# Kernel tuning notes

Measured on AMD Instinct MI355X. Metric: run time of the kernel, lower is better.

Reference implementation:

```python
import jax, jax.numpy as jnp
import numpy as np

D = 128          # embed_dim
NSYM = 100000    # num_symbols
PAD = NSYM       # padding index
DM = 2 * D       # d_model for support/query encoders
HID = 2 * DM     # LSTMCell hidden size
STEPS = 4        # process_steps
K_NEI = 10       # k_neighbors
EPS = 1e-8
LN_EPS = 1e-5
SLOPE = 0.01     # F.leaky_relu default negative slope


def _neighbor_encoder(conn, num_neighbors, self_ids, sym_emb, gcn_w_W, gcn_w_b, gcn_b, gate_w, gate_temp):
    rel = conn[..., 0]                      # [N, K]
    ent = conn[..., 1]                      # [N, K]
    rel_e = sym_emb[rel]                    # [N, K, D]  (dropout is identity in eval)
    ent_e = sym_emb[ent]                    # [N, K, D]
    self_e = sym_emb[self_ids]              # [N, D]
    concat = jnp.concatenate([rel_e, ent_e], axis=-1)                 # [N, K, 2D]
    proj = jax.nn.leaky_relu(concat @ gcn_w_W.T + gcn_w_b + gcn_b, SLOPE)
    proj = proj * (rel != PAD)[..., None].astype(proj.dtype)          # zero padded slots
    d = D // 2
    rs, is_ = self_e[:, None, :d], self_e[:, None, d:]
    rn, in_ = proj[..., :d], proj[..., d:]
    num = jnp.sum(rs * rn, -1) + jnp.sum(is_ * in_, -1)               # [N, K]
    n_self = jnp.sqrt(jnp.sum(rs * rs + is_ * is_, -1) + EPS)
    n_nei = jnp.sqrt(jnp.sum(rn * rn + in_ * in_, -1) + EPS)
    cos = num / (n_self * n_nei + EPS)
    _, idx = jax.lax.top_k(cos, K_NEI)                                # [N, k]
    agg = jnp.take_along_axis(proj, idx[..., None], axis=1).mean(axis=1)   # [N, D]
    rel_ids = jnp.where(rel == PAD, 0, rel)
    gate = jax.nn.sigmoid(gate_w[rel_ids, 0].mean(axis=1, keepdims=True) / gate_temp)  # [N, 1]
    gate = jnp.where(num_neighbors[:, None] > 0, gate, jnp.ones_like(gate))
    return jnp.tanh(self_e + gate * agg)


def _support_encoder(x, W1, b1, W2, b2, g, b):
    # FFN with residual + LayerNorm (dropout = identity in eval)
    h = jax.nn.relu(x @ W1.T + b1) @ W2.T + b2 + x
    mu = h.mean(-1, keepdims=True)
    var = ((h - mu) ** 2).mean(-1, keepdims=True)
    return g * (h - mu) / jnp.sqrt(var + LN_EPS) + b


def _query_encoder(support, query, Wih, Whh, bih, bhh):
    # Matching-network process block: LSTMCell attention over support
    B = query.shape[0]
    h_r = jnp.zeros((B, HID), query.dtype)
    c = jnp.zeros((B, HID), query.dtype)
    h = query
    for _ in range(STEPS):  # small fixed loop
        gates = query @ Wih.T + bih + h_r @ Whh.T + bhh
        i, f, g, o = jnp.split(gates, 4, axis=-1)
        c = jax.nn.sigmoid(f) * c + jax.nn.sigmoid(i) * jnp.tanh(g)
        h_new = jax.nn.sigmoid(o) * jnp.tanh(c)
        h = query + h_new[:, :DM]
        attn = jax.nn.softmax(h @ support.T, axis=1)
        r = attn @ support
        h_r = jnp.concatenate([h, r], axis=1)
    return h


def _forward(query, support, q_l1, q_deg_l, q_r1, q_deg_r, s_l1, s_deg_l, s_r1, s_deg_r, p):
    ne = lambda conn, deg, ids: _neighbor_encoder(conn, deg, ids, p['sym_emb'], p['gcn_w_W'], p['gcn_w_b'], p['gcn_b'], p['gate_w'], p['gate_temp'])
    q_vec = jnp.concatenate([ne(q_l1, q_deg_l, query[:, 0]), ne(q_r1, q_deg_r, query[:, 1])], -1)   # [B, DM]
    s_vec = jnp.concatenate([ne(s_l1, s_deg_l, support[:, 0]), ne(s_r1, s_deg_r, support[:, 1])], -1)
    se = lambda x: _support_encoder(x, p['se_W1'], p['se_b1'], p['se_W2'], p['se_b2'], p['ln_g'], p['ln_b'])
    support_g = se(s_vec).mean(axis=0, keepdims=True)   # [1, DM]
    query_enc = se(q_vec)                                # [B, DM]
    query_g = _query_encoder(support_g, query_enc, p['lstm_Wih'], p['lstm_Whh'], p['lstm_bih'], p['lstm_bhh'])
    d = DM // 2
    rq, iq = query_g[..., :d], query_g[..., d:]
    rs, is_ = support_g[..., :d], support_g[..., d:]
    num = jnp.sum(rq * rs, -1) + jnp.sum(iq * is_, -1)
    den = jnp.sqrt(jnp.sum(rq * rq + iq * iq, -1) + EPS) * jnp.sqrt(jnp.sum(rs * rs + is_ * is_, -1) + EPS)
    return num / den  # [B]


def setup_inputs():
    key = jax.random.key(0)
    ks = jax.random.split(key, 24)
    B, FEW, MAXK = 4096, 5, 50
    ri = lambda k, shp, hi: jax.random.randint(k, shp, 0, hi)
    inp = dict(
        query=ri(ks[0], (B, 2), NSYM),
        support=ri(ks[1], (FEW, 2), NSYM),
        q_l1=ri(ks[2], (B, MAXK, 2), NSYM + 1),
        q_deg_l=ri(ks[3], (B,), MAXK),
        q_r1=ri(ks[4], (B, MAXK, 2), NSYM + 1),
        q_deg_r=ri(ks[5], (B,), MAXK),
        s_l1=ri(ks[6], (FEW, MAXK, 2), NSYM + 1),
        s_deg_l=ri(ks[7], (FEW,), MAXK),
        s_r1=ri(ks[8], (FEW, MAXK, 2), NSYM + 1),
        s_deg_r=ri(ks[9], (FEW,), MAXK),
    )
    xav = lambda k, shp: jax.random.normal(k, shp) * np.float32(np.sqrt(2.0 / (shp[0] + shp[1])))
    sym = jax.random.normal(ks[10], (NSYM + 1, D)) * 0.02
    inp['sym_emb'] = sym.at[PAD].set(0.0)
    inp['gcn_w_W'] = xav(ks[11], (D, 2 * D))
    inp['gcn_w_b'] = jnp.zeros((D,))
    inp['gcn_b'] = jnp.zeros((D,))
    inp['gate_w'] = 1.0 + 0.05 * jax.random.normal(ks[12], (NSYM, 1))
    inp['gate_temp'] = jnp.asarray(1.0, jnp.float32)
    inp['se_W1'] = xav(ks[13], (2 * DM, DM))
    inp['se_b1'] = jnp.zeros((2 * DM,))
    inp['se_W2'] = xav(ks[14], (DM, 2 * DM))
    inp['se_b2'] = jnp.zeros((DM,))
    inp['ln_g'] = jnp.ones((DM,))
    inp['ln_b'] = jnp.zeros((DM,))
    s = float(1.0 / np.sqrt(HID))
    u = lambda k, shp: jax.random.uniform(k, shp, minval=-s, maxval=s)
    inp['lstm_Wih'] = u(ks[15], (4 * HID, DM))
    inp['lstm_Whh'] = u(ks[16], (4 * HID, HID))
    inp['lstm_bih'] = u(ks[17], (4 * HID,))
    inp['lstm_bhh'] = u(ks[18], (4 * HID,))
    return inp


def reference(query, support, q_l1, q_deg_l, q_r1, q_deg_r, s_l1, s_deg_l, s_r1, s_deg_r,
              sym_emb, gcn_w_W, gcn_w_b, gcn_b, gate_w, gate_temp,
              se_W1, se_b1, se_W2, se_b2, ln_g, ln_b,
              lstm_Wih, lstm_Whh, lstm_bih, lstm_bhh):
    p = dict(sym_emb=sym_emb, gcn_w_W=gcn_w_W, gcn_w_b=gcn_w_b, gcn_b=gcn_b, gate_w=gate_w,
             gate_temp=gate_temp, se_W1=se_W1, se_b1=se_b1, se_W2=se_W2, se_b2=se_b2,
             ln_g=ln_g, ln_b=ln_b, lstm_Wih=lstm_Wih, lstm_Whh=lstm_Whh, lstm_bih=lstm_bih, lstm_bhh=lstm_bhh)
    return _forward(query, support, q_l1, q_deg_l, q_r1, q_deg_r, s_l1, s_deg_l, s_r1, s_deg_r, p)
```

## Files before the change

### kernel.cpp

```cpp
#include <hip/hip_runtime.h>

#define PADID  100000
#define DEPS   1e-8f
#define LNEPS  1e-5f

typedef unsigned short u16;
typedef unsigned int u32;
typedef __attribute__((ext_vector_type(8))) short s16x8;
typedef __attribute__((ext_vector_type(4))) float f32x4;

__device__ __forceinline__ float sigm(float x) { return 1.f / (1.f + expf(-x)); }
__device__ __forceinline__ float bf2f(u16 v) { return __uint_as_float(((u32)v) << 16); }
__device__ __forceinline__ u16 f2bf(float f) {
    u32 x = __float_as_uint(f);
    x += 0x7FFFu + ((x >> 16) & 1u);
    return (u16)(x >> 16);
}

__global__ void transpose_f32(const float* __restrict__ src, float* __restrict__ dst,
                              int R, int C) {
    int idx = blockIdx.x * 256 + threadIdx.x;
    if (idx < R * C) {
        int r = idx / C, c = idx - r * C;
        dst[c * R + r] = src[idx];
    }
}

__global__ __launch_bounds__(256) void ne_kernel(
    const float* __restrict__ sym, const float* __restrict__ wT,
    const float* __restrict__ wbias, const float* __restrict__ gbias,
    const float* __restrict__ gate_w, const float* __restrict__ gtemp,
    const int* __restrict__ query, const int* __restrict__ support,
    const int* __restrict__ q_l1, const int* __restrict__ q_r1,
    const int* __restrict__ s_l1, const int* __restrict__ s_r1,
    const int* __restrict__ q_deg_l, const int* __restrict__ q_deg_r,
    const int* __restrict__ s_deg_l, const int* __restrict__ s_deg_r,
    float* __restrict__ qvec, float* __restrict__ svec)
{
    const int bid  = blockIdx.x;
    const int row  = bid >> 1;
    const int side = bid & 1;
    const int t    = threadIdx.x;
    const int tk   = t & 15;
    const int tj   = t >> 4;

    const int* conn; int selfid, deg; float* out;
    if (row < 4096) {
        conn   = (side ? q_r1 : q_l1) + row * 100;
        deg    = (side ? q_deg_r : q_deg_l)[row];
        selfid = query[row * 2 + side];
        out    = qvec + row * 256 + side * 128;
    } else {
        int r  = row - 4096;
        conn   = (side ? s_r1 : s_l1) + r * 100;
        deg    = (side ? s_deg_r : s_deg_l)[r];
        selfid = support[r * 2 + side];
        out    = svec + r * 256 + side * 128;
    }

    __shared__ float s_nei[64][66];
    __shared__ float s_agg[16][132];
    __shared__ int   s_rel[50], s_ent[50];
    __shared__ float s_self[128];
    __shared__ float s_cos[64];
    __shared__ int   s_topk[10];
    __shared__ float s_misc[2];

    if (t < 50) { s_rel[t] = conn[2 * t]; s_ent[t] = conn[2 * t + 1]; }
    if (t < 128) s_self[t] = sym[(size_t)selfid * 128 + t];
    __syncthreads();

    float sf[8];
    #pragma unroll
    for (int e = 0; e < 8; ++e) sf[e] = s_self[tk * 8 + e];
    if (t < 64) {
        float a = s_self[t], b = s_self[t + 64];
        float s2 = a * a + b * b;
        #pragma unroll
        for (int off = 32; off; off >>= 1) s2 += __shfl_xor(s2, off);
        if (t == 0) s_misc[0] = s2;
    }

    float acc[4][8];
    #pragma unroll
    for (int m = 0; m < 4; ++m)
        #pragma unroll
        for (int e = 0; e < 8; ++e) acc[m][e] = 0.f;

    for (int c = 0; c < 4; ++c) {
        for (int idx = t; idx < 64 * 16; idx += 256) {
            int j = idx >> 4, k4 = (idx & 15) * 4;
            float4 v = make_float4(0.f, 0.f, 0.f, 0.f);
            if (j < 50) {
                int kin = c * 64 + k4;
                int id  = (kin < 128) ? s_rel[j] : s_ent[j];
                v = *(const float4*)&sym[(size_t)id * 128 + (kin & 127)];
            }
            *(float4*)&s_nei[j][k4] = v;
        }
        __syncthreads();
        #pragma unroll 2
        for (int k2 = 0; k2 < 64; ++k2) {
            const float* wrow = wT + (size_t)(c * 64 + k2) * 128 + tk * 8;
            float4 wv0 = *(const float4*)wrow;
            float4 wv1 = *(const float4*)(wrow + 4);
            float wv[8] = {wv0.x, wv0.y, wv0.z, wv0.w, wv1.x, wv1.y, wv1.z, wv1.w};
            #pragma unroll
            for (int m = 0; m < 4; ++m) {
                float nv = s_nei[tj + m * 16][k2];
                #pragma unroll
                for (int e = 0; e < 8; ++e) acc[m][e] += nv * wv[e];
            }
        }
        __syncthreads();
    }

    float wsum[8];
    #pragma unroll
    for (int e = 0; e < 8; ++e) {
        int k = tk * 8 + e;
        wsum[e] = wbias[k] + gbias[k];
    }
    #pragma unroll
    for (int m = 0; m < 4; ++m) {
        int j = tj + m * 16;
        bool dead = (j >= 50) || (s_rel[j < 50 ? j : 0] == PADID && j < 50);
        #pragma unroll
        for (int e = 0; e < 8; ++e) {
            float v = acc[m][e] + wsum[e];
            v = (v > 0.f) ? v : 0.01f * v;
            acc[m][e] = dead ? 0.f : v;
        }
    }

    {
        float ns = sqrtf(s_misc[0] + DEPS);
        #pragma unroll
        for (int m = 0; m < 4; ++m) {
            float num = 0.f, nn = 0.f;
            #pragma unroll
            for (int e = 0; e < 8; ++e) {
                float pv = acc[m][e];
                num += pv * sf[e];
                nn  += pv * pv;
            }
            #pragma unroll
            for (int off = 1; off < 16; off <<= 1) {
                num += __shfl_xor(num, off);
                nn  += __shfl_xor(nn,  off);
            }
            if (tk == 0) {
                int j = tj + m * 16;
                if (j < 50) s_cos[j] = num / (ns * sqrtf(nn + DEPS) + DEPS);
            }
        }
    }
    __syncthreads();

    if (t < 64) {
        float myv  = (t < 50) ? s_cos[t] : -3.4e38f;
        int   live = (t < 50) ? 1 : 0;
        for (int m = 0; m < 10; ++m) {
            float bv = live ? myv : -3.4e38f;
            int   bi = t;
            #pragma unroll
            for (int off = 1; off < 64; off <<= 1) {
                float ov = __shfl_xor(bv, off);
                int   oi = __shfl_xor(bi, off);
                if (ov > bv || (ov == bv && oi < bi)) { bv = ov; bi = oi; }
            }
            if (bi == t) live = 0;
            if (t == 0) s_topk[m] = bi;
        }
        float g = 0.f;
        if (t < 50) {
            int r = s_rel[t];
            g = gate_w[(r == PADID) ? 0 : r];
        }
        #pragma unroll
        for (int off = 32; off; off >>= 1) g += __shfl_xor(g, off);
        if (t == 0) {
            float gate = sigm((g / 50.f) / gtemp[0]);
            if (deg <= 0) gate = 1.f;
            s_misc[1] = gate;
        }
    }
    __syncthreads();

    {
        float ag[8];
        #pragma unroll
        for (int e = 0; e < 8; ++e) ag[e] = 0.f;
        #pragma unroll
        for (int m = 0; m < 4; ++m) {
            int j = tj + m * 16;
            bool sel = false;
            #pragma unroll
            for (int m2 = 0; m2 < 10; ++m2) sel |= (s_topk[m2] == j);
            if (sel)
                #pragma unroll
                for (int e = 0; e < 8; ++e) ag[e] += acc[m][e];
        }
        *(float4*)&s_agg[tj][tk * 8]     = make_float4(ag[0], ag[1], ag[2], ag[3]);
        *(float4*)&s_agg[tj][tk * 8 + 4] = make_float4(ag[4], ag[5], ag[6], ag[7]);
    }
    __syncthreads();

    if (t < 128) {
        float a = 0.f;
        #pragma unroll
        for (int r = 0; r < 16; ++r) a += s_agg[r][t];
        a *= 0.1f;
        out[t] = tanhf(s_self[t] + s_misc[1] * a);
    }
}

#define SE_ROWS 4
__global__ __launch_bounds__(256) void se_kernel(
    const float* __restrict__ qvec, const float* __restrict__ svec,
    const float* __restrict__ w1T, const float* __restrict__ w2T,
    const float* __restrict__ b1, const float* __restrict__ b2,
    const float* __restrict__ lng, const float* __restrict__ lnb,
    float* __restrict__ qenc, float* __restrict__ senc)
{
    const int t  = threadIdx.x;
    const int r0 = blockIdx.x * SE_ROWS;

    __shared__ float sx[SE_ROWS][256];
    __shared__ float shid[SE_ROWS][512];
    __shared__ float sred[4][SE_ROWS][2];

    for (int idx = t; idx < SE_ROWS * 64; idx += 256) {
        int r = idx >> 6, k4 = (idx & 63) * 4;
        int row = r0 + r;
        float4 v = make_float4(0.f, 0.f, 0.f, 0.f);
        if (row < 4101) {
            const float* x = (row < 4096) ? (qvec + (size_t)row * 256)
                                          : (svec + (size_t)(row - 4096) * 256);
            v = *(const float4*)&x[k4];
        }
        *(float4*)&sx[r][k4] = v;
    }
    __syncthreads();

    float h[2][SE_ROWS];
    {
        float bb0 = b1[t], bb1 = b1[t + 256];
        #pragma unroll
        for (int r = 0; r < SE_ROWS; ++r) { h[0][r] = bb0; h[1][r] = bb1; }
    }
    for (int k = 0; k < 256; ++k) {
        float w0 = w1T[k * 512 + t];
        float w1 = w1T[k * 512 + t + 256];
        #pragma unroll
        for (int r = 0; r < SE_ROWS; ++r) {
            float xv = sx[r][k];
            h[0][r] += xv * w0;
            h[1][r] += xv * w1;
        }
    }
    #pragma unroll
    for (int r = 0; r < SE_ROWS; ++r) {
        shid[r][t]       = fmaxf(h[0][r], 0.f);
        shid[r][t + 256] = fmaxf(h[1][r], 0.f);
    }
    __syncthreads();

    float acc2[SE_ROWS];
    {
        float bb = b2[t];
        #pragma unroll
        for (int r = 0; r < SE_ROWS; ++r) acc2[r] = bb + sx[r][t];
    }
    for (int k = 0; k < 512; ++k) {
        float w = w2T[k * 256 + t];
        #pragma unroll
        for (int r = 0; r < SE_ROWS; ++r) acc2[r] += shid[r][k] * w;
    }

    int wv = t >> 6;
    #pragma unroll
    for (int r = 0; r < SE_ROWS; ++r) {
        float s = acc2[r], q = acc2[r] * acc2[r];
        #pragma unroll
        for (int off = 32; off; off >>= 1) {
            s += __shfl_xor(s, off);
            q += __shfl_xor(q, off);
        }
        if ((t & 63) == 0) { sred[wv][r][0] = s; sred[wv][r][1] = q; }
    }
    __syncthreads();
    float gv = lng[t], bv = lnb[t];
    #pragma unroll
    for (int r = 0; r < SE_ROWS; ++r) {
        int row = r0 + r;
        if (row < 4101) {
            float S = sred[0][r][0] + sred[1][r][0] + sred[2][r][0] + sred[3][r][0];
            float Q = sred[0][r][1] + sred[1][r][1] + sred[2][r][1] + sred[3][r][1];
            float mu  = S / 256.f;
            float var = Q / 256.f - mu * mu;
            float o = gv * (acc2[r] - mu) / sqrtf(var + LNEPS) + bv;
            float* op = (row < 4096) ? (qenc + (size_t)row * 256)
                                     : (senc + (size_t)(row - 4096) * 256);
            op[t] = o;
        }
    }
}

__global__ __launch_bounds__(256) void supg_kernel(
    const float* __restrict__ senc, float* __restrict__ supg,
    float* __restrict__ ssqp)
{
    int t = threadIdx.x;
    __shared__ float sr[4];
    float m = (senc[t] + senc[256 + t] + senc[512 + t] + senc[768 + t] + senc[1024 + t]) * 0.2f;
    supg[t] = m;
    float sq = m * m;
    #pragma unroll
    for (int off = 32; off; off >>= 1) sq += __shfl_xor(sq, off);
    if ((t & 63) == 0) sr[t >> 6] = sq;
    __syncthreads();
    if (t == 0) ssqp[0] = sr[0] + sr[1] + sr[2] + sr[3];
}

__global__ __launch_bounds__(256) void supc_kernel(
    const float* __restrict__ supg, const float* __restrict__ Whh,
    const float* __restrict__ bih, const float* __restrict__ bhh,
    float* __restrict__ supc0, float* __restrict__ supc)
{
    const int t = threadIdx.x, w = t >> 6, l = t & 63;
    __shared__ float sg[256];
    if (t < 256) sg[t] = supg[t];
    __syncthreads();
    float4 gv = *(const float4*)&sg[l * 4];
    #pragma unroll
    for (int jj = 0; jj < 16; ++jj) {
        int j = blockIdx.x * 64 + w * 16 + jj;
        float4 wv = *(const float4*)&Whh[(size_t)j * 512 + 256 + l * 4];
        float p = gv.x * wv.x + gv.y * wv.y + gv.z * wv.z + gv.w * wv.w;
        #pragma unroll
        for (int off = 32; off; off >>= 1) p += __shfl_xor(p, off);
        if (l == 0) {
            float c0 = bih[j] + bhh[j];
            supc0[j] = c0;
            supc[j]  = c0 + p;
        }
    }
}

__global__ __launch_bounds__(256) void prep_kernel(
    const float* __restrict__ qenc, const float* __restrict__ Wih,
    const float* __restrict__ Whh, u16* __restrict__ Abf, u16* __restrict__ Wcat)
{
    int idx = blockIdx.x * 256 + threadIdx.x;
    if (idx < 1048576) {
        int m = idx >> 8, k = idx & 255;
        Abf[(size_t)m * 512 + k] = f2bf(qenc[idx]);
    } else if (idx < 1572864) {
        int i = idx - 1048576;
        int n = i >> 8, k = i & 255;
        Wcat[(size_t)n * 512 + k] = f2bf(Wih[i]);
    } else {
        int i = idx - 1572864;
        int n = i >> 8, k = i & 255;
        Wcat[(size_t)n * 512 + 256 + k] = f2bf(Whh[(size_t)n * 512 + k]);
    }
}

__global__ __launch_bounds__(256) void lstm_mfma(
    const u16* __restrict__ A, const u16* __restrict__ B,
    u16* __restrict__ C, int Klen)
{
    __shared__ u16 sA[64][72];
    __shared__ u16 sB[64][72];
    const int t    = threadIdx.x;
    const int wid  = t >> 6;
    const int lane = t & 63;
    const int m0   = blockIdx.x * 64;
    const int n0   = blockIdx.y * 64;
    const int mw   = (wid & 1) * 32;
    const int nw   = (wid >> 1) * 32;
    const int r    = t >> 2;
    const int q    = t & 3;
    const int fr   = lane & 15;
    const int fk   = (lane >> 4) * 8;

    f32x4 acc[2][2];
    #pragma unroll
    for (int i = 0; i < 2; ++i)
        #pragma unroll
        for (int j = 0; j < 2; ++j)
            acc[i][j] = (f32x4){0.f, 0.f, 0.f, 0.f};

    for (int k0 = 0; k0 < Klen; k0 += 64) {
        const u16* ga = A + (size_t)(m0 + r) * 512 + k0 + q * 16;
        const u16* gb = B + (size_t)(n0 + r) * 512 + k0 + q * 16;
        uint4 va0 = *(const uint4*)ga;
        uint4 va1 = *(const uint4*)(ga + 8);
        uint4 vb0 = *(const uint4*)gb;
        uint4 vb1 = *(const uint4*)(gb + 8);
        __syncthreads();
        *(uint4*)&sA[r][q * 16]     = va0;
        *(uint4*)&sA[r][q * 16 + 8] = va1;
        *(uint4*)&sB[r][q * 16]     = vb0;
        *(uint4*)&sB[r][q * 16 + 8] = vb1;
        __syncthreads();
        #pragma unroll
        for (int ks = 0; ks < 64; ks += 32) {
            s16x8 af[2], bf[2];
            #pragma unroll
            for (int i = 0; i < 2; ++i)
                af[i] = *(const s16x8*)&sA[mw + i * 16 + fr][ks + fk];
            #pragma unroll
            for (int j = 0; j < 2; ++j)
                bf[j] = *(const s16x8*)&sB[nw + j * 16 + fr][ks + fk];
            #pragma unroll
            for (int i = 0; i < 2; ++i)
                #pragma unroll
                for (int j = 0; j < 2; ++j)
                    acc[i][j] = __builtin_amdgcn_mfma_f32_16x16x32_bf16(
                        af[i], bf[j], acc[i][j], 0, 0, 0);
        }
    }

    #pragma unroll
    for (int i = 0; i < 2; ++i)
        #pragma unroll
        for (int j = 0; j < 2; ++j) {
            int col = n0 + nw + j * 16 + fr;
            #pragma unroll
            for (int rr = 0; rr < 4; ++rr) {
                int rowi = m0 + mw + i * 16 + (lane >> 4) * 4 + rr;
                C[(size_t)rowi * 2048 + col] = f2bf(acc[i][j][rr]);
            }
        }
}

__global__ __launch_bounds__(256) void lstm_elem(
    const u16* __restrict__ gates, const float* __restrict__ cvec,
    float* __restrict__ cbuf, const float* __restrict__ qenc,
    u16* __restrict__ Abf, float* __restrict__ hfinal, int step)
{
    int idx = blockIdx.x * 256 + threadIdx.x;
    int m = idx >> 9, j = idx & 511;
    const u16* g = gates + (size_t)m * 2048;
    float iv = bf2f(g[j])        + cvec[j];
    float fv = bf2f(g[512 + j])  + cvec[512 + j];
    float gv = bf2f(g[1024 + j]) + cvec[1024 + j];
    float ov = bf2f(g[1536 + j]) + cvec[1536 + j];
    float cold = (step == 0) ? 0.f : cbuf[idx];
    float cn = sigm(fv) * cold + sigm(iv) * tanhf(gv);
    cbuf[idx] = cn;
    if (j < 256) {
        float hn = sigm(ov) * tanhf(cn);
        float h  = qenc[(size_t)m * 256 + j] + hn;
        Abf[(size_t)m * 512 + 256 + j] = f2bf(h);
        if (step == 3) hfinal[(size_t)m * 256 + j] = h;
    }
}

__global__ __launch_bounds__(256) void final_kernel(
    const float* __restrict__ h, const float* __restrict__ supg,
    const float* __restrict__ ssqp, float* __restrict__ outp)
{
    int t = threadIdx.x;
    int w = t >> 6, l = t & 63;
    int b = blockIdx.x * 4 + w;
    float4 q = *(const float4*)&h[b * 256 + l * 4];
    float4 s = *(const float4*)&supg[l * 4];
    float num = q.x * s.x + q.y * s.y + q.z * s.z + q.w * s.w;
    float qq  = q.x * q.x + q.y * q.y + q.z * q.z + q.w * q.w;
    #pragma unroll
    for (int off = 32; off; off >>= 1) {
        num += __shfl_xor(num, off);
        qq  += __shfl_xor(qq,  off);
    }
    if (l == 0) {
        float den = sqrtf(qq + DEPS) * sqrtf(ssqp[0] + DEPS);
        outp[b] = num / den;
    }
}

extern "C" void kernel_launch(void* const* d_in, const int* in_sizes, int n_in,
                              void* d_out, int out_size, void* d_ws, size_t ws_size,
                              hipStream_t stream) {
    const int* query      = (const int*)d_in[0];
    const int* support    = (const int*)d_in[1];
    const int* q_l1       = (const int*)d_in[2];
    const int* q_deg_l    = (const int*)d_in[3];
    const int* q_r1       = (const int*)d_in[4];
    const int* q_deg_r    = (const int*)d_in[5];
    const int* s_l1       = (const int*)d_in[6];
    const int* s_deg_l    = (const int*)d_in[7];
    const int* s_r1       = (const int*)d_in[8];
    const int* s_deg_r    = (const int*)d_in[9];
    const float* sym      = (const float*)d_in[10];
    const float* gcn_w_W  = (const float*)d_in[11];
    const float* gcn_w_b  = (const float*)d_in[12];
    const float* gcn_b    = (const float*)d_in[13];
    const float* gate_w   = (const float*)d_in[14];
    const float* gtemp    = (const float*)d_in[15];
    const float* se_W1    = (const float*)d_in[16];
    const float* se_b1    = (const float*)d_in[17];
    const float* se_W2    = (const float*)d_in[18];
    const float* se_b2    = (const float*)d_in[19];
    const float* ln_g     = (const float*)d_in[20];
    const float* ln_b     = (const float*)d_in[21];
    const float* lstm_Wih = (const float*)d_in[22];
    const float* lstm_Whh = (const float*)d_in[23];
    const float* lstm_bih = (const float*)d_in[24];
    const float* lstm_bhh = (const float*)d_in[25];

    float* ws    = (float*)d_ws;
    float* qvec  = ws;
    float* qenc  = qvec  + 1048576;
    float* h1    = qenc  + 1048576;
    float* cbuf  = h1    + 1048576;
    float* svec  = cbuf  + 2097152;
    float* senc  = svec  + 1280;
    float* supg  = senc  + 1280;
    float* supc0 = supg  + 256;
    float* supc  = supc0 + 2048;
    float* ssqp  = supc  + 2048;
    float* wT    = h1;
    float* w1T   = h1 + 32768;
    float* w2T   = h1 + 163840;
    float* h0    = qvec;
    float* bfbase = ssqp + 64;
    u16* Abf  = (u16*)bfbase;
    u16* Wcat = Abf + 2097152;
    u16* gates= Wcat + 1048576;

    transpose_f32<<<128, 256, 0, stream>>>(gcn_w_W, wT, 128, 256);
    transpose_f32<<<512, 256, 0, stream>>>(se_W1, w1T, 512, 256);
    transpose_f32<<<512, 256, 0, stream>>>(se_W2, w2T, 256, 512);

    ne_kernel<<<8202, 256, 0, stream>>>(
        sym, wT, gcn_w_b, gcn_b, gate_w, gtemp,
        query, support, q_l1, q_r1, s_l1, s_r1,
        q_deg_l, q_deg_r, s_deg_l, s_deg_r, qvec, svec);

    se_kernel<<<1026, 256, 0, stream>>>(
        qvec, svec, w1T, w2T, se_b1, se_b2, ln_g, ln_b, qenc, senc);

    prep_kernel<<<8192, 256, 0, stream>>>(qenc, lstm_Wih, lstm_Whh, Abf, Wcat);
    supg_kernel<<<1, 256, 0, stream>>>(senc, supg, ssqp);
    supc_kernel<<<32, 256, 0, stream>>>(supg, lstm_Whh, lstm_bih, lstm_bhh, supc0, supc);

    for (int s = 0; s < 4; ++s) {
        lstm_mfma<<<dim3(64, 32), 256, 0, stream>>>(Abf, Wcat, gates, s == 0 ? 256 : 512);
        lstm_elem<<<8192, 256, 0, stream>>>(gates, s == 0 ? supc0 : supc,
                                            cbuf, qenc, Abf, h0, s);
    }

    final_kernel<<<1024, 256, 0, stream>>>(h0, supg, ssqp, (float*)d_out);
}
```

Before: 847.1 us.

## Move neighbor-encoder projection onto bf16 MFMA with three-way split precision

Replaces the scalar FP32 GEMM in the neighbor encoder with MFMA bf16 instructions. Both the gathered embeddings and the weights are split into high, mid and low bf16 parts, and six cross-products are summed to approximate FP32 accuracy. Each block now handles two entity rows (128 neighbor slots) and uses a swizzled LDS layout. The weight split is precomputed by a new kernel. The change targets the FP32 ALU cost of the projection, at the price of extra conversion work and more LDS, which may lower occupancy.

```diff
diff --git a/kernel.cpp b/kernel.cpp
--- a/kernel.cpp
+++ b/kernel.cpp
@@ -26,8 +26,20 @@
     }
 }
 
-__global__ __launch_bounds__(256) void ne_kernel(
-    const float* __restrict__ sym, const float* __restrict__ wT,
+__global__ void wsplit_kernel(const float* __restrict__ W, u16* __restrict__ wh,
+                              u16* __restrict__ wm, u16* __restrict__ wl) {
+    int idx = blockIdx.x * 256 + threadIdx.x;
+    float x = W[idx];
+    u16 h = f2bf(x);  float hf = __uint_as_float((u32)h << 16);
+    float r1 = x - hf;
+    u16 m = f2bf(r1); float mf = __uint_as_float((u32)m << 16);
+    u16 l2 = f2bf(r1 - mf);
+    wh[idx] = h; wm[idx] = m; wl[idx] = l2;
+}
+
+__global__ __launch_bounds__(256) void ne_mfma(
+    const float* __restrict__ sym,
+    const u16* __restrict__ wh, const u16* __restrict__ wm, const u16* __restrict__ wl,
     const float* __restrict__ wbias, const float* __restrict__ gbias,
     const float* __restrict__ gate_w, const float* __restrict__ gtemp,
     const int* __restrict__ query, const int* __restrict__ support,
@@ -37,181 +49,265 @@
     const int* __restrict__ s_deg_l, const int* __restrict__ s_deg_r,
     float* __restrict__ qvec, float* __restrict__ svec)
 {
-    const int bid  = blockIdx.x;
-    const int row  = bid >> 1;
-    const int side = bid & 1;
-    const int t    = threadIdx.x;
-    const int tk   = t & 15;
-    const int tj   = t >> 4;
-
-    const int* conn; int selfid, deg; float* out;
-    if (row < 4096) {
-        conn   = (side ? q_r1 : q_l1) + row * 100;
-        deg    = (side ? q_deg_r : q_deg_l)[row];
-        selfid = query[row * 2 + side];
-        out    = qvec + row * 256 + side * 128;
-    } else {
-        int r  = row - 4096;
-        conn   = (side ? s_r1 : s_l1) + r * 100;
-        deg    = (side ? s_deg_r : s_deg_l)[r];
-        selfid = support[r * 2 + side];
-        out    = svec + r * 256 + side * 128;
-    }
-
-    __shared__ float s_nei[64][66];
-    __shared__ float s_agg[16][132];
-    __shared__ int   s_rel[50], s_ent[50];
-    __shared__ float s_self[128];
-    __shared__ float s_cos[64];
-    __shared__ int   s_topk[10];
-    __shared__ float s_misc[2];
-
-    if (t < 50) { s_rel[t] = conn[2 * t]; s_ent[t] = conn[2 * t + 1]; }
-    if (t < 128) s_self[t] = sym[(size_t)selfid * 128 + t];
-    __syncthreads();
-
-    float sf[8];
-    #pragma unroll
-    for (int e = 0; e < 8; ++e) sf[e] = s_self[tk * 8 + e];
-    if (t < 64) {
-        float a = s_self[t], b = s_self[t + 64];
+    __shared__ __align__(16) u16 sAb[3][128 * 64];
+    __shared__ float s_self[2][128];
+    __shared__ int   s_idr[128], s_ide[128];
+    __shared__ float s_mask[128];
+    __shared__ float s_norm[2];
+    float* s_red  = (float*)&sAb[0][0];
+    float* s_cosA = s_red + 512;
+    int*   s_topk = (int*)(s_cosA + 128);
+    float* s_gate = (float*)(s_topk + 20);
+
+    const int t = threadIdx.x;
+    const int w = t >> 6, l = t & 63;
+    const int fr = l & 15, fq = l >> 4;
+
+    int selfid[2], deg[2];
+    const int* conn[2];
+    float* outp[2];
+    #pragma unroll
+    for (int u = 0; u < 2; ++u) {
+        int gu = blockIdx.x * 2 + u;
+        int row = gu >> 1, side = gu & 1;
+        if (row < 4096) {
+            conn[u]   = (side ? q_r1 : q_l1) + row * 100;
+            deg[u]    = (side ? q_deg_r : q_deg_l)[row];
+            selfid[u] = query[row * 2 + side];
+            outp[u]   = qvec + (size_t)row * 256 + side * 128;
+        } else {
+            int r = row - 4096;
+            conn[u]   = (side ? s_r1 : s_l1) + r * 100;
+            deg[u]    = (side ? s_deg_r : s_deg_l)[r];
+            selfid[u] = support[r * 2 + side];
+            outp[u]   = svec + (size_t)r * 256 + side * 128;
+        }
+    }
+
+    if (t < 128) {
+        int u = t >> 6, jj = t & 63;
+        int ir = 0, ie = 0; float mk = 0.f;
+        if (jj < 50) {
+            ir = conn[u][2 * jj]; ie = conn[u][2 * jj + 1];
+            mk = (ir == PADID) ? 0.f : 1.f;
+        }
+        s_idr[t] = ir; s_ide[t] = ie; s_mask[t] = mk;
+    }
+    { int u = t >> 7, d = t & 127;
+      s_self[u][d] = sym[(size_t)selfid[u] * 128 + d]; }
+    if (w < 2) {
+        float a = s_self[w][l], b = s_self[w][l + 64];
         float s2 = a * a + b * b;
         #pragma unroll
         for (int off = 32; off; off >>= 1) s2 += __shfl_xor(s2, off);
-        if (t == 0) s_misc[0] = s2;
-    }
-
-    float acc[4][8];
-    #pragma unroll
-    for (int m = 0; m < 4; ++m)
-        #pragma unroll
-        for (int e = 0; e < 8; ++e) acc[m][e] = 0.f;
+        if (l == 0) s_norm[w] = s2;
+    }
+
+    f32x4 acc[4][4];
+    #pragma unroll
+    for (int mt = 0; mt < 4; ++mt)
+        #pragma unroll
+        for (int nt = 0; nt < 4; ++nt)
+            acc[mt][nt] = (f32x4){0.f, 0.f, 0.f, 0.f};
+
+    const int rbase = (w >> 1) * 64;
+    const int cbase = (w & 1) * 64;
+    const u16* wt0[3] = {wh, wm, wl};
 
     for (int c = 0; c < 4; ++c) {
-        for (int idx = t; idx < 64 * 16; idx += 256) {
-            int j = idx >> 4, k4 = (idx & 15) * 4;
-            float4 v = make_float4(0.f, 0.f, 0.f, 0.f);
-            if (j < 50) {
-                int kin = c * 64 + k4;
-                int id  = (kin < 128) ? s_rel[j] : s_ent[j];
-                v = *(const float4*)&sym[(size_t)id * 128 + (kin & 127)];
-            }
-            *(float4*)&s_nei[j][k4] = v;
-        }
         __syncthreads();
-        #pragma unroll 2
-        for (int k2 = 0; k2 < 64; ++k2) {
-            const float* wrow = wT + (size_t)(c * 64 + k2) * 128 + tk * 8;
-            float4 wv0 = *(const float4*)wrow;
-            float4 wv1 = *(const float4*)(wrow + 4);
-            float wv[8] = {wv0.x, wv0.y, wv0.z, wv0.w, wv1.x, wv1.y, wv1.z, wv1.w};
-            #pragma unroll
-            for (int m = 0; m < 4; ++m) {
-                float nv = s_nei[tj + m * 16][k2];
+        #pragma unroll
+        for (int i = 0; i < 4; ++i) {
+            int seg = i * 256 + t;
+            int r = seg >> 3, kc = seg & 7;
+            int id = (c < 2) ? s_idr[r] : s_ide[r];
+            int scol = (c & 1) * 64 + kc * 8;
+            const float* src = sym + (size_t)id * 128 + scol;
+            float x[8];
+            *(float4*)&x[0] = *(const float4*)src;
+            *(float4*)&x[4] = *(const float4*)(src + 4);
+            u16 hh_[8], mm_[8], ll_[8];
+            #pragma unroll
+            for (int e = 0; e < 8; ++e) {
+                float xv = x[e];
+                u16 h = f2bf(xv);  float hf = __uint_as_float((u32)h << 16);
+                float r1 = xv - hf;
+                u16 m = f2bf(r1);  float mf = __uint_as_float((u32)m << 16);
+                u16 l2 = f2bf(r1 - mf);
+                hh_[e] = h; mm_[e] = m; ll_[e] = l2;
+            }
+            int didx = r * 64 + ((kc ^ (r & 7)) * 8);
+            uint4 ph, pm, pl;
+            ph.x = hh_[0] | ((u32)hh_[1] << 16); ph.y = hh_[2] | ((u32)hh_[3] << 16);
+            ph.z = hh_[4] | ((u32)hh_[5] << 16); ph.w = hh_[6] | ((u32)hh_[7] << 16);
+            pm.x = mm_[0] | ((u32)mm_[1] << 16); pm.y = mm_[2] | ((u32)mm_[3] << 16);
+            pm.z = mm_[4] | ((u32)mm_[5] << 16); pm.w = mm_[6] | ((u32)mm_[7] << 16);
+            pl.x = ll_[0] | ((u32)ll_[1] << 16); pl.y = ll_[2] | ((u32)ll_[3] << 16);
+            pl.z = ll_[4] | ((u32)ll_[5] << 16); pl.w = ll_[6] | ((u32)ll_[7] << 16);
+            *(uint4*)&sAb[0][didx] = ph;
+            *(uint4*)&sAb[1][didx] = pm;
+            *(uint4*)&sAb[2][didx] = pl;
+        }
+        __syncthreads();
+        #pragma unroll
+        for (int s2 = 0; s2 < 2; ++s2) {
+            int gnu = s2 * 4 + fq;
+            int kin = c * 64 + s2 * 32 + fq * 8;
+            #pragma unroll
+            for (int sb = 0; sb < 3; ++sb) {
+                s16x8 bfr[4];
                 #pragma unroll
-                for (int e = 0; e < 8; ++e) acc[m][e] += nv * wv[e];
-            }
-        }
-        __syncthreads();
-    }
-
-    float wsum[8];
-    #pragma unroll
-    for (int e = 0; e < 8; ++e) {
-        int k = tk * 8 + e;
-        wsum[e] = wbias[k] + gbias[k];
-    }
-    #pragma unroll
-    for (int m = 0; m < 4; ++m) {
-        int j = tj + m * 16;
-        bool dead = (j >= 50) || (s_rel[j < 50 ? j : 0] == PADID && j < 50);
-        #pragma unroll
-        for (int e = 0; e < 8; ++e) {
-            float v = acc[m][e] + wsum[e];
-            v = (v > 0.f) ? v : 0.01f * v;
-            acc[m][e] = dead ? 0.f : v;
-        }
-    }
-
-    {
-        float ns = sqrtf(s_misc[0] + DEPS);
-        #pragma unroll
-        for (int m = 0; m < 4; ++m) {
-            float num = 0.f, nn = 0.f;
-            #pragma unroll
-            for (int e = 0; e < 8; ++e) {
-                float pv = acc[m][e];
-                num += pv * sf[e];
-                nn  += pv * pv;
-            }
-            #pragma unroll
-            for (int off = 1; off < 16; off <<= 1) {
-                num += __shfl_xor(num, off);
-                nn  += __shfl_xor(nn,  off);
-            }
-            if (tk == 0) {
-                int j = tj + m * 16;
-                if (j < 50) s_cos[j] = num / (ns * sqrtf(nn + DEPS) + DEPS);
-            }
-        }
-    }
-    __syncthreads();
-
-    if (t < 64) {
-        float myv  = (t < 50) ? s_cos[t] : -3.4e38f;
-        int   live = (t < 50) ? 1 : 0;
+                for (int nt = 0; nt < 4; ++nt) {
+                    int col = cbase + nt * 16 + fr;
+                    bfr[nt] = *(const s16x8*)(wt0[sb] + (size_t)col * 256 + kin);
+                }
+                #pragma unroll
+                for (int sa = 0; sa < 3 - sb; ++sa) {
+                    s16x8 af[4];
+                    #pragma unroll
+                    for (int mt = 0; mt < 4; ++mt) {
+                        int rowi = rbase + mt * 16 + fr;
+                        af[mt] = *(const s16x8*)&sAb[sa][rowi * 64 + ((gnu ^ (rowi & 7)) * 8)];
+                    }
+                    #pragma unroll
+                    for (int mt = 0; mt < 4; ++mt)
+                        #pragma unroll
+                        for (int nt = 0; nt < 4; ++nt)
+                            acc[mt][nt] = __builtin_amdgcn_mfma_f32_16x16x32_bf16(
+                                af[mt], bfr[nt], acc[mt][nt], 0, 0, 0);
+                }
+            }
+        }
+    }
+    __syncthreads();
+
+    const int u = w >> 1;
+    float biasc[4], sfv[4];
+    #pragma unroll
+    for (int nt = 0; nt < 4; ++nt) {
+        int jc = cbase + nt * 16 + fr;
+        biasc[nt] = wbias[jc] + gbias[jc];
+        sfv[nt]   = s_self[u][jc];
+    }
+    float msk[4][4];
+    #pragma unroll
+    for (int mt = 0; mt < 4; ++mt)
+        #pragma unroll
+        for (int rr = 0; rr < 4; ++rr)
+            msk[mt][rr] = s_mask[rbase + mt * 16 + fq * 4 + rr];
+    #pragma unroll
+    for (int mt = 0; mt < 4; ++mt)
+        #pragma unroll
+        for (int nt = 0; nt < 4; ++nt)
+            #pragma unroll
+            for (int rr = 0; rr < 4; ++rr) {
+                float v = acc[mt][nt][rr] + biasc[nt];
+                v = (v > 0.f) ? v : 0.01f * v;
+                acc[mt][nt][rr] = v * msk[mt][rr];
+            }
+
+    #pragma unroll
+    for (int mt = 0; mt < 4; ++mt)
+        #pragma unroll
+        for (int rr = 0; rr < 4; ++rr) {
+            float np_ = 0.f, nn_ = 0.f;
+            #pragma unroll
+            for (int nt = 0; nt < 4; ++nt) {
+                float v = acc[mt][nt][rr];
+                np_ += v * sfv[nt];
+                nn_ += v * v;
+            }
+            np_ += __shfl_xor(np_, 1); nn_ += __shfl_xor(nn_, 1);
+            np_ += __shfl_xor(np_, 2); nn_ += __shfl_xor(nn_, 2);
+            np_ += __shfl_xor(np_, 4); nn_ += __shfl_xor(nn_, 4);
+            np_ += __shfl_xor(np_, 8); nn_ += __shfl_xor(nn_, 8);
+            if (fr == 0) {
+                int j = mt * 16 + fq * 4 + rr;
+                float* rp = s_red + (u * 64 + j) * 4 + (w & 1) * 2;
+                rp[0] = np_; rp[1] = nn_;
+            }
+        }
+    __syncthreads();
+
+    if (t < 128) {
+        int uu = t >> 6;
+        float num = s_red[t * 4 + 0] + s_red[t * 4 + 2];
+        float nn  = s_red[t * 4 + 1] + s_red[t * 4 + 3];
+        float ns  = sqrtf(s_norm[uu] + DEPS);
+        s_cosA[t] = num / (ns * sqrtf(nn + DEPS) + DEPS);
+    }
+    __syncthreads();
+
+    if ((w & 1) == 0) {
+        int uu = w >> 1;
+        float myv = (l < 50) ? s_cosA[uu * 64 + l] : -3.4e38f;
+        int live  = (l < 50) ? 1 : 0;
         for (int m = 0; m < 10; ++m) {
             float bv = live ? myv : -3.4e38f;
-            int   bi = t;
+            int   bi = l;
             #pragma unroll
             for (int off = 1; off < 64; off <<= 1) {
                 float ov = __shfl_xor(bv, off);
                 int   oi = __shfl_xor(bi, off);
                 if (ov > bv || (ov == bv && oi < bi)) { bv = ov; bi = oi; }
             }
-            if (bi == t) live = 0;
-            if (t == 0) s_topk[m] = bi;
-        }
+            if (bi == l) live = 0;
+            if (l == 0) s_topk[uu * 10 + m] = bi;
+        }
+    } else {
+        int uu = w >> 1;
         float g = 0.f;
-        if (t < 50) {
-            int r = s_rel[t];
+        if (l < 50) {
+            int r = s_idr[uu * 64 + l];
             g = gate_w[(r == PADID) ? 0 : r];
         }
         #pragma unroll
         for (int off = 32; off; off >>= 1) g += __shfl_xor(g, off);
-        if (t == 0) {
+        if (l == 0) {
             float gate = sigm((g / 50.f) / gtemp[0]);
-            if (deg <= 0) gate = 1.f;
-            s_misc[1] = gate;
+            if (deg[uu] <= 0) gate = 1.f;
+            s_gate[uu] = gate;
         }
     }
     __syncthreads();
 
     {
-        float ag[8];
-        #pragma unroll
-        for (int e = 0; e < 8; ++e) ag[e] = 0.f;
-        #pragma unroll
-        for (int m = 0; m < 4; ++m) {
-            int j = tj + m * 16;
-            bool sel = false;
-            #pragma unroll
-            for (int m2 = 0; m2 < 10; ++m2) sel |= (s_topk[m2] == j);
-            if (sel)
+        bool sel[4][4];
+        #pragma unroll
+        for (int mt = 0; mt < 4; ++mt)
+            #pragma unroll
+            for (int rr = 0; rr < 4; ++rr) sel[mt][rr] = false;
+        #pragma unroll
+        for (int i2 = 0; i2 < 10; ++i2) {
+            int tj = s_topk[u * 10 + i2];
+            #pragma unroll
+            for (int mt = 0; mt < 4; ++mt)
                 #pragma unroll
-                for (int e = 0; e < 8; ++e) ag[e] += acc[m][e];
-        }
-        *(float4*)&s_agg[tj][tk * 8]     = make_float4(ag[0], ag[1], ag[2], ag[3]);
-        *(float4*)&s_agg[tj][tk * 8 + 4] = make_float4(ag[4], ag[5], ag[6], ag[7]);
-    }
-    __syncthreads();
-
-    if (t < 128) {
-        float a = 0.f;
-        #pragma unroll
-        for (int r = 0; r < 16; ++r) a += s_agg[r][t];
-        a *= 0.1f;
-        out[t] = tanhf(s_self[t] + s_misc[1] * a);
+                for (int rr = 0; rr < 4; ++rr)
+                    sel[mt][rr] = sel[mt][rr] | (mt * 16 + fq * 4 + rr == tj);
+        }
+        float ag[4] = {0.f, 0.f, 0.f, 0.f};
+        #pragma unroll
+        for (int mt = 0; mt < 4; ++mt)
+            #pragma unroll
+            for (int rr = 0; rr < 4; ++rr)
+                if (sel[mt][rr]) {
+                    #pragma unroll
+                    for (int nt = 0; nt < 4; ++nt) ag[nt] += acc[mt][nt][rr];
+                }
+        #pragma unroll
+        for (int nt = 0; nt < 4; ++nt) {
+            ag[nt] += __shfl_xor(ag[nt], 16);
+            ag[nt] += __shfl_xor(ag[nt], 32);
+        }
+        if (fq == 0) {
+            float gate = s_gate[u];
+            #pragma unroll
+            for (int nt = 0; nt < 4; ++nt) {
+                int jc = cbase + nt * 16 + fr;
+                outp[u][jc] = tanhf(s_self[u][jc] + gate * ag[nt] * 0.1f);
+            }
+        }
     }
 }
 
@@ -522,21 +618,23 @@
     float* supc0 = supg  + 256;
     float* supc  = supc0 + 2048;
     float* ssqp  = supc  + 2048;
-    float* wT    = h1;
-    float* w1T   = h1 + 32768;
-    float* w2T   = h1 + 163840;
+    float* w1T   = h1;
+    float* w2T   = h1 + 131072;
     float* h0    = qvec;
     float* bfbase = ssqp + 64;
-    u16* Abf  = (u16*)bfbase;
-    u16* Wcat = Abf + 2097152;
-    u16* gates= Wcat + 1048576;
-
-    transpose_f32<<<128, 256, 0, stream>>>(gcn_w_W, wT, 128, 256);
+    u16* Abf   = (u16*)bfbase;
+    u16* Wcat  = Abf + 2097152;
+    u16* gates = Wcat + 1048576;
+    u16* wh    = gates + 8388608;
+    u16* wmS   = wh + 32768;
+    u16* wlS   = wmS + 32768;
+
     transpose_f32<<<512, 256, 0, stream>>>(se_W1, w1T, 512, 256);
     transpose_f32<<<512, 256, 0, stream>>>(se_W2, w2T, 256, 512);
-
-    ne_kernel<<<8202, 256, 0, stream>>>(
-        sym, wT, gcn_w_b, gcn_b, gate_w, gtemp,
+    wsplit_kernel<<<128, 256, 0, stream>>>(gcn_w_W, wh, wmS, wlS);
+
+    ne_mfma<<<4101, 256, 0, stream>>>(
+        sym, wh, wmS, wlS, gcn_w_b, gcn_b, gate_w, gtemp,
         query, support, q_l1, q_r1, s_l1, s_r1,
         q_deg_l, q_deg_r, s_deg_l, s_deg_r, qvec, svec);
 
```

New measurement: 695.0 us. 17.9% less time.
